# Optimization experiments

Hardware: AMD Instinct MI355X
Metric: run time of the kernel (lower is better)

Reference implementation:

```python
import jax, jax.numpy as jnp
import numpy as np

EPS = 1e-9

def _cheb_attention_conv(X_real, X_imag, lap_real, lap_imag,
                         Wa_real, Wa_imag, ba_real, ba_imag,
                         modrelu_b, W_real, W_imag):
    B, N, C = X_real.shape
    # --- attention scores: CVLinear over cat([x_i, x_j]) == (X@W1)_i + (X@W2)_j + b ---
    W1r, W2r = Wa_real[:C, 0], Wa_real[C:, 0]  # [C]
    W1i, W2i = Wa_imag[:C, 0], Wa_imag[C:, 0]
    # complex matvec: (Xr + iXi)(Wr + iWi)
    si_r = X_real @ W1r - X_imag @ W1i          # [B,N] contribution of x_i
    si_i = X_real @ W1i + X_imag @ W1r
    sj_r = X_real @ W2r - X_imag @ W2i          # [B,N] contribution of x_j
    sj_i = X_real @ W2i + X_imag @ W2r
    sc_r = si_r[:, :, None] + sj_r[:, None, :] + ba_real[0]   # [B,N,N]
    sc_i = si_i[:, :, None] + sj_i[:, None, :] + ba_imag[0]
    # --- learnable modReLU: relu(|z| + b) * z/|z| ---
    mag = jnp.sqrt(sc_r * sc_r + sc_i * sc_i)
    scale = jax.nn.relu(mag + modrelu_b[0]) / (mag + EPS)
    sc_r = sc_r * scale
    sc_i = sc_i * scale
    # --- split complex softmax over last dim ---
    a_r = jax.nn.softmax(sc_r, axis=-1)
    a_i = jax.nn.softmax(sc_i, axis=-1)
    # --- reweight Laplacian polynomials (complex mult, broadcast over k) ---
    L_r = lap_real * a_r[:, None] - lap_imag * a_i[:, None]   # [B,K+1,N,N]
    L_i = lap_real * a_i[:, None] + lap_imag * a_r[:, None]
    # --- sum_k (L_k X) W_k, complex ---
    LX_r = jnp.einsum('bkij,bjc->bkic', L_r, X_real) - jnp.einsum('bkij,bjc->bkic', L_i, X_imag)
    LX_i = jnp.einsum('bkij,bjc->bkic', L_r, X_imag) + jnp.einsum('bkij,bjc->bkic', L_i, X_real)
    out_r = jnp.einsum('bkic,kco->bio', LX_r, W_real) - jnp.einsum('bkic,kco->bio', LX_i, W_imag)
    out_i = jnp.einsum('bkic,kco->bio', LX_r, W_imag) + jnp.einsum('bkic,kco->bio', LX_i, W_real)
    return out_r, out_i


def setup_inputs() -> dict:
    key = jax.random.key(0)
    ks = jax.random.split(key, 8)
    B, N, C, CO, K1 = 48, 512, 64, 64, 5
    # weights normalized to unit complex magnitude like the torch init
    wr = jax.random.uniform(ks[4], (K1, C, CO), minval=-1.0, maxval=1.0) / np.sqrt(CO)
    wi = jax.random.uniform(ks[5], (K1, C, CO), minval=-1.0, maxval=1.0) / np.sqrt(CO)
    m = jnp.sqrt(wr * wr + wi * wi)
    return {
        'X_real': jax.random.normal(ks[0], (B, N, C), jnp.float32),
        'X_imag': jax.random.normal(ks[1], (B, N, C), jnp.float32),
        'lap_real': jax.random.normal(ks[2], (B, K1, N, N), jnp.float32) * 0.1,
        'lap_imag': jax.random.normal(ks[3], (B, K1, N, N), jnp.float32) * 0.1,
        'Wa_real': jax.random.normal(ks[6], (2 * C, 1), jnp.float32) * 0.1,
        'Wa_imag': jax.random.normal(ks[7], (2 * C, 1), jnp.float32) * 0.1,
        'ba_real': jnp.zeros((1,), jnp.float32),
        'ba_imag': jnp.zeros((1,), jnp.float32),
        'modrelu_b': jnp.zeros((1,), jnp.float32),
        'W_real': (wr / m).astype(jnp.float32),
        'W_imag': (wi / m).astype(jnp.float32),
    }


def reference(X_real, X_imag, lap_real, lap_imag, Wa_real, Wa_imag,
              ba_real, ba_imag, modrelu_b, W_real, W_imag):
    out_r, out_i = _cheb_attention_conv(X_real, X_imag, lap_real, lap_imag,
                                        Wa_real, Wa_imag, ba_real, ba_imag,
                                        modrelu_b, W_real, W_imag)
    return out_r, out_i
```

## Files before the change

### kernel.cpp

```cpp
#include <hip/hip_runtime.h>

#define EPSF 1e-9f

typedef __attribute__((ext_vector_type(8))) short short8;
typedef __attribute__((ext_vector_type(4))) float f32x4;
typedef __attribute__((ext_vector_type(4))) unsigned int u32x4;
typedef __attribute__((ext_vector_type(2))) unsigned int u32x2;

__device__ __forceinline__ unsigned pkbf(float lo, float hi) {
  unsigned r;
  asm("v_cvt_pk_bf16_f32 %0, %1, %2" : "=v"(r) : "v"(lo), "v"(hi));
  return r;
}
__device__ __forceinline__ short8 mk8(unsigned a, unsigned b, unsigned c, unsigned d) {
  u32x4 u = {a, b, c, d};
  return __builtin_bit_cast(short8, u);
}

__global__ __launch_bounds__(256) void k_s(
    const float* __restrict__ Xr, const float* __restrict__ Xi,
    const float* __restrict__ War, const float* __restrict__ Wai,
    float4* __restrict__ s4, float2* __restrict__ sj2)
{
  int t = threadIdx.x;
  int nf = blockIdx.x * 32 + (t >> 3);
  int c0 = (t & 7) * 8;
  const f32x4* xr = (const f32x4*)(Xr + (size_t)nf * 64 + c0);
  const f32x4* xi = (const f32x4*)(Xi + (size_t)nf * 64 + c0);
  const f32x4* w1r = (const f32x4*)(War + c0);
  const f32x4* w2r = (const f32x4*)(War + 64 + c0);
  const f32x4* w1i = (const f32x4*)(Wai + c0);
  const f32x4* w2i = (const f32x4*)(Wai + 64 + c0);
  float sir = 0.f, sii = 0.f, sjr = 0.f, sji = 0.f;
#pragma unroll
  for (int h = 0; h < 2; ++h) {
    f32x4 a = xr[h], bb = xi[h];
    f32x4 u1r = w1r[h], u1i = w1i[h], u2r = w2r[h], u2i = w2i[h];
#pragma unroll
    for (int e = 0; e < 4; ++e) {
      sir += a[e] * u1r[e] - bb[e] * u1i[e];
      sii += a[e] * u1i[e] + bb[e] * u1r[e];
      sjr += a[e] * u2r[e] - bb[e] * u2i[e];
      sji += a[e] * u2i[e] + bb[e] * u2r[e];
    }
  }
#pragma unroll
  for (int off = 1; off < 8; off <<= 1) {
    sir += __shfl_xor(sir, off);
    sii += __shfl_xor(sii, off);
    sjr += __shfl_xor(sjr, off);
    sji += __shfl_xor(sji, off);
  }
  if ((t & 7) == 0) {
    s4[nf] = make_float4(sir, sii, sjr, sji);
    sj2[nf] = make_float2(sjr, sji);
  }
}

__global__ __launch_bounds__(256) void k_stats(
    const float4* __restrict__ s4, const float2* __restrict__ sj2,
    const float* __restrict__ bar, const float* __restrict__ bai,
    const float* __restrict__ modbp, float4* __restrict__ stats)
{
  __shared__ float2 sh[512];
  int t = threadIdx.x;
  int b = blockIdx.x >> 4;
  int i0 = (blockIdx.x & 15) * 32;
  sh[t] = sj2[(size_t)b * 512 + t];
  sh[t + 256] = sj2[(size_t)b * 512 + t + 256];
  __syncthreads();
  float ba_r = bar[0], ba_i = bai[0], modb = modbp[0];
  int i = i0 + (t >> 3), jl = t & 7;
  float4 sv = s4[(size_t)b * 512 + i];
  float sirb = sv.x + ba_r, siib = sv.y + ba_i;
  float mr = -1e30f, mi = -1e30f;
  for (int jj = 0; jj < 64; ++jj) {
    float2 sj = sh[jl * 64 + jj];
    float scr = sirb + sj.x, sci = siib + sj.y;
    float mag = sqrtf(scr * scr + sci * sci);
    float sc = fmaxf(mag + modb, 0.f) * __builtin_amdgcn_rcpf(mag + EPSF);
    mr = fmaxf(mr, scr * sc);
    mi = fmaxf(mi, sci * sc);
  }
#pragma unroll
  for (int off = 1; off < 8; off <<= 1) {
    mr = fmaxf(mr, __shfl_xor(mr, off));
    mi = fmaxf(mi, __shfl_xor(mi, off));
  }
  float er = 0.f, ei = 0.f;
  for (int jj = 0; jj < 64; ++jj) {
    float2 sj = sh[jl * 64 + jj];
    float scr = sirb + sj.x, sci = siib + sj.y;
    float mag = sqrtf(scr * scr + sci * sci);
    float sc = fmaxf(mag + modb, 0.f) * __builtin_amdgcn_rcpf(mag + EPSF);
    er += __expf(scr * sc - mr);
    ei += __expf(sci * sc - mi);
  }
#pragma unroll
  for (int off = 1; off < 8; off <<= 1) {
    er += __shfl_xor(er, off);
    ei += __shfl_xor(ei, off);
  }
  if (jl == 0)
    stats[(size_t)b * 512 + i] = make_float4(mr, 1.f / er, mi, 1.f / ei);
}

__global__ __launch_bounds__(256) void k_y(
    const float* __restrict__ Xr, const float* __restrict__ Xi,
    const float* __restrict__ Wr, const float* __restrict__ Wi,
    u32x4* __restrict__ yfrag)
{
  __shared__ __align__(16) short WtR[64 * 72];
  __shared__ __align__(16) short WtI[64 * 72];
  __shared__ __align__(16) short Yt[4][2][64 * 24];
  int bk = blockIdx.x;
  int b = bk / 5, k = bk % 5;
  int t = threadIdx.x;
  {
    int o = t & 63, cbase = (t >> 6) * 16;
    const float* wr = Wr + (size_t)k * 4096;
    const float* wi = Wi + (size_t)k * 4096;
#pragma unroll
    for (int cc = 0; cc < 16; cc += 2) {
      int c = cbase + cc;
      *(unsigned*)&WtR[o * 72 + c] = pkbf(wr[c * 64 + o], wr[(c + 1) * 64 + o]);
      *(unsigned*)&WtI[o * 72 + c] = pkbf(wi[c * 64 + o], wi[(c + 1) * 64 + o]);
    }
  }
  __syncthreads();
  int w = t >> 6, l = t & 63;
  int lane15 = l & 15, quad = l >> 4;
  short* ytR = &Yt[w][0][0];
  short* ytI = &Yt[w][1][0];
  for (int qq = 0; qq < 8; ++qq) {
    int q = w * 8 + qq;
    int j = q * 16 + lane15;
    const f32x4* pxr = (const f32x4*)(Xr + ((size_t)b * 512 + j) * 64 + quad * 8);
    const f32x4* pxi = (const f32x4*)(Xi + ((size_t)b * 512 + j) * 64 + quad * 8);
    f32x4 xr0 = pxr[0], xr1 = pxr[1], xr8 = pxr[8], xr9 = pxr[9];
    f32x4 xi0 = pxi[0], xi1 = pxi[1], xi8 = pxi[8], xi9 = pxi[9];
    short8 axr[2], axi[2];
    axr[0] = mk8(pkbf(xr0[0], xr0[1]), pkbf(xr0[2], xr0[3]), pkbf(xr1[0], xr1[1]), pkbf(xr1[2], xr1[3]));
    axr[1] = mk8(pkbf(xr8[0], xr8[1]), pkbf(xr8[2], xr8[3]), pkbf(xr9[0], xr9[1]), pkbf(xr9[2], xr9[3]));
    axi[0] = mk8(pkbf(xi0[0], xi0[1]), pkbf(xi0[2], xi0[3]), pkbf(xi1[0], xi1[1]), pkbf(xi1[2], xi1[3]));
    axi[1] = mk8(pkbf(xi8[0], xi8[1]), pkbf(xi8[2], xi8[3]), pkbf(xi9[0], xi9[1]), pkbf(xi9[2], xi9[3]));
    f32x4 aR1[4], aR2[4], aI[4];
#pragma unroll
    for (int os = 0; os < 4; ++os) {
      aR1[os] = f32x4{0.f, 0.f, 0.f, 0.f};
      aR2[os] = f32x4{0.f, 0.f, 0.f, 0.f};
      aI[os] = f32x4{0.f, 0.f, 0.f, 0.f};
    }
#pragma unroll
    for (int kc = 0; kc < 2; ++kc) {
#pragma unroll
      for (int os = 0; os < 4; ++os) {
        int widx = (os * 16 + lane15) * 72 + kc * 32 + quad * 8;
        short8 wrF = *(const short8*)&WtR[widx];
        short8 wiF = *(const short8*)&WtI[widx];
        aR1[os] = __builtin_amdgcn_mfma_f32_16x16x32_bf16(axr[kc], wrF, aR1[os], 0, 0, 0);
        aR2[os] = __builtin_amdgcn_mfma_f32_16x16x32_bf16(axi[kc], wiF, aR2[os], 0, 0, 0);
        aI[os]  = __builtin_amdgcn_mfma_f32_16x16x32_bf16(axr[kc], wiF, aI[os], 0, 0, 0);
        aI[os]  = __builtin_amdgcn_mfma_f32_16x16x32_bf16(axi[kc], wrF, aI[os], 0, 0, 0);
      }
    }
#pragma unroll
    for (int os = 0; os < 4; ++os) {
      f32x4 R = aR1[os] - aR2[os];
      f32x4 I = aI[os];
      int ya = (os * 16 + lane15) * 24 + quad * 4;
      *(u32x2*)&ytR[ya] = u32x2{pkbf(R[0], R[1]), pkbf(R[2], R[3])};
      *(u32x2*)&ytI[ya] = u32x2{pkbf(I[0], I[1]), pkbf(I[2], I[3])};
    }
#pragma unroll
    for (int part = 0; part < 2; ++part) {
      const short* yt = part ? ytI : ytR;
#pragma unroll
      for (int h = 0; h < 2; ++h) {
        short8 unit = *(const short8*)&yt[l * 24 + h * 8];
        size_t line = (((size_t)(b * 5 + k) * 2 + part) * 16 + (q >> 1)) * 4 + (l >> 4);
        size_t idx = line * 64 + ((q & 1) * 2 + h) * 16 + (l & 15);
        yfrag[idx] = __builtin_bit_cast(u32x4, unit);
      }
    }
  }
}

__global__ __launch_bounds__(256) __attribute__((amdgpu_waves_per_eu(2, 2)))
void k_main(
    const float* __restrict__ lapr, const float* __restrict__ lapi,
    const float4* __restrict__ s4, const float4* __restrict__ stats,
    const float2* __restrict__ sj2, const u32x4* __restrict__ yfrag,
    const float* __restrict__ bar, const float* __restrict__ bai,
    const float* __restrict__ modbp,
    float* __restrict__ out_r, float* __restrict__ out_i)
{
  __shared__ __align__(16) f32x4 red[2][64][8];

  const int g = blockIdx.x;
  const int b = (g & 7) + ((g >> 8) << 3);
  const int it = (g >> 3) & 31;
  const int t = threadIdx.x;
  const int w = t >> 6;
  const int l = t & 63;
  const int lane15 = l & 15, quad = l >> 4;
  const int gi = it * 16 + lane15;

  float ba_r = bar[0], ba_i = bai[0], modb = modbp[0];
  float4 sv = s4[(size_t)b * 512 + gi];
  float4 st = stats[(size_t)b * 512 + gi];
  float sirb = sv.x + ba_r, siib = sv.y + ba_i;
  float maxr = st.x, rsr = st.y, maxi = st.z, rsi = st.w;

  f32x4 accR[4], accI[4];
#pragma unroll
  for (int os = 0; os < 4; ++os) {
    accR[os] = f32x4{0.f, 0.f, 0.f, 0.f};
    accI[os] = f32x4{0.f, 0.f, 0.f, 0.f};
  }

  const size_t NN = (size_t)512 * 512;
  const float* lapr_b = lapr + ((size_t)b * 5 * 512 + gi) * 512;
  const float* lapi_b = lapi + ((size_t)b * 5 * 512 + gi) * 512;
  const u32x4* yb = yfrag + (size_t)b * 5 * 8192 + l;

  for (int jsw = 0; jsw < 4; ++jsw) {
    const int js = w * 4 + jsw;
    const int jq = js * 32 + quad * 8;

    const f32x4* sjp = (const f32x4*)(sj2 + (size_t)b * 512 + jq);
    f32x4 sjv0 = sjp[0], sjv1 = sjp[1], sjv2 = sjp[2], sjv3 = sjp[3];

    f32x4 LR[5][2], LI[5][2];
#pragma unroll
    for (int k = 0; k < 5; ++k) {
      const f32x4* pr = (const f32x4*)(lapr_b + (size_t)k * NN + jq);
      const f32x4* pi_ = (const f32x4*)(lapi_b + (size_t)k * NN + jq);
      LR[k][0] = __builtin_nontemporal_load(pr);
      LR[k][1] = __builtin_nontemporal_load(pr + 1);
      LI[k][0] = __builtin_nontemporal_load(pi_);
      LI[k][1] = __builtin_nontemporal_load(pi_ + 1);
    }
    __builtin_amdgcn_sched_barrier(0);

    float sjr[8] = {sjv0[0], sjv0[2], sjv1[0], sjv1[2], sjv2[0], sjv2[2], sjv3[0], sjv3[2]};
    float sjimag[8] = {sjv0[1], sjv0[3], sjv1[1], sjv1[3], sjv2[1], sjv2[3], sjv3[1], sjv3[3]};
    float ar[8], ai[8];
#pragma unroll
    for (int e = 0; e < 8; ++e) {
      float scr = sirb + sjr[e];
      float sci = siib + sjimag[e];
      float mag = __builtin_amdgcn_sqrtf(fmaf(scr, scr, sci * sci));
      float sc = fmaxf(mag + modb, 0.f) * __builtin_amdgcn_rcpf(mag + EPSF);
      ar[e] = __expf(fmaf(scr, sc, -maxr)) * rsr;
      ai[e] = __expf(fmaf(sci, sc, -maxi)) * rsi;
    }

#pragma unroll
    for (int k = 0; k < 5; ++k) {
      float lrv[8], liv[8];
#pragma unroll
      for (int e = 0; e < 4; ++e) {
        lrv[e]     = LR[k][0][e] * ar[e]     - LI[k][0][e] * ai[e];
        liv[e]     = LR[k][0][e] * ai[e]     + LI[k][0][e] * ar[e];
        lrv[4 + e] = LR[k][1][e] * ar[4 + e] - LI[k][1][e] * ai[4 + e];
        liv[4 + e] = LR[k][1][e] * ai[4 + e] + LI[k][1][e] * ar[4 + e];
      }
      unsigned p0 = pkbf(lrv[0], lrv[1]), p1 = pkbf(lrv[2], lrv[3]);
      unsigned p2 = pkbf(lrv[4], lrv[5]), p3 = pkbf(lrv[6], lrv[7]);
      unsigned q0 = pkbf(liv[0], liv[1]), q1 = pkbf(liv[2], liv[3]);
      unsigned q2 = pkbf(liv[4], liv[5]), q3 = pkbf(liv[6], liv[7]);
      short8 Ar = mk8(p0, p1, p2, p3);
      short8 Ai = mk8(q0, q1, q2, q3);
      short8 An = mk8(q0 ^ 0x80008000u, q1 ^ 0x80008000u,
                      q2 ^ 0x80008000u, q3 ^ 0x80008000u);

      const u32x4* yk = yb + (size_t)k * 8192 + (size_t)(js * 4) * 64;
#pragma unroll
      for (int os = 0; os < 4; ++os) {
        short8 br8 = __builtin_bit_cast(short8, yk[os * 64]);
        short8 bi8 = __builtin_bit_cast(short8, yk[4096 + os * 64]);
        accR[os] = __builtin_amdgcn_mfma_f32_16x16x32_bf16(Ar, br8, accR[os], 0, 0, 0);
        accR[os] = __builtin_amdgcn_mfma_f32_16x16x32_bf16(An, bi8, accR[os], 0, 0, 0);
        accI[os] = __builtin_amdgcn_mfma_f32_16x16x32_bf16(Ar, bi8, accI[os], 0, 0, 0);
        accI[os] = __builtin_amdgcn_mfma_f32_16x16x32_bf16(Ai, br8, accI[os], 0, 0, 0);
      }
    }
  }

  if (w >= 2) {
#pragma unroll
    for (int os = 0; os < 4; ++os) {
      red[w - 2][l][os] = accR[os];
      red[w - 2][l][4 + os] = accI[os];
    }
  }
  __syncthreads();
  if (w < 2) {
#pragma unroll
    for (int os = 0; os < 4; ++os) {
      accR[os] += red[w][l][os];
      accI[os] += red[w][l][4 + os];
    }
  }
  __syncthreads();
  if (w == 1) {
#pragma unroll
    for (int os = 0; os < 4; ++os) {
      red[0][l][os] = accR[os];
      red[0][l][4 + os] = accI[os];
    }
  }
  __syncthreads();
  if (w == 0) {
#pragma unroll
    for (int os = 0; os < 4; ++os) {
      accR[os] += red[0][l][os];
      accI[os] += red[0][l][4 + os];
      int oc = os * 16 + lane15;
#pragma unroll
      for (int r = 0; r < 4; ++r) {
        size_t oidx = ((size_t)b * 512 + it * 16 + quad * 4 + r) * 64 + oc;
        out_r[oidx] = accR[os][r];
        out_i[oidx] = accI[os][r];
      }
    }
  }
}

extern "C" void kernel_launch(void* const* d_in, const int* in_sizes, int n_in,
                              void* d_out, int out_size, void* d_ws, size_t ws_size,
                              hipStream_t stream) {
  const float* Xr = (const float*)d_in[0];
  const float* Xi = (const float*)d_in[1];
  const float* lapr = (const float*)d_in[2];
  const float* lapi = (const float*)d_in[3];
  const float* War = (const float*)d_in[4];
  const float* Wai = (const float*)d_in[5];
  const float* bar = (const float*)d_in[6];
  const float* bai = (const float*)d_in[7];
  const float* modb = (const float*)d_in[8];
  const float* Wr = (const float*)d_in[9];
  const float* Wi = (const float*)d_in[10];

  char* wsb = (char*)d_ws;
  float4* s4 = (float4*)wsb;
  float4* stats = (float4*)(wsb + 393216);
  float2* sj2 = (float2*)(wsb + 786432);
  u32x4* yfrag = (u32x4*)(wsb + 983040);

  float* out_r = (float*)d_out;
  float* out_i = out_r + (size_t)48 * 512 * 64;

  k_s<<<768, 256, 0, stream>>>(Xr, Xi, War, Wai, s4, sj2);
  k_stats<<<768, 256, 0, stream>>>(s4, sj2, bar, bai, modb, stats);
  k_y<<<240, 256, 0, stream>>>(Xr, Xi, Wr, Wi, yfrag);
  k_main<<<1536, 256, 0, stream>>>(lapr, lapi, s4, stats, sj2, yfrag,
                                   bar, bai, modb, out_r, out_i);
}
```

Before: 190.8 us.

## Relax waves-per-eu, use plain Laplacian loads, and make reduction buffer scalar-strided

Three unrelated tweaks to the main kernel. The waves_per_eu attribute goes from (2,2) to (2,8), so the compiler may use fewer registers and allow more resident waves. The Laplacian loads switch from nontemporal to ordinary cached loads. The shared-memory reduction buffer becomes a scalar-per-lane layout, trading wide 16-byte LDS accesses for conflict-free 4-byte ones. Higher occupancy could add register pressure or spills, and cached loads may pollute the cache for streamed data.

```diff
diff --git a/kernel.cpp b/kernel.cpp
--- a/kernel.cpp
+++ b/kernel.cpp
@@ -186,7 +186,7 @@
   }
 }
 
-__global__ __launch_bounds__(256) __attribute__((amdgpu_waves_per_eu(2, 2)))
+__global__ __launch_bounds__(256) __attribute__((amdgpu_waves_per_eu(2, 8)))
 void k_main(
     const float* __restrict__ lapr, const float* __restrict__ lapi,
     const float4* __restrict__ s4, const float4* __restrict__ stats,
@@ -195,7 +195,7 @@
     const float* __restrict__ modbp,
     float* __restrict__ out_r, float* __restrict__ out_i)
 {
-  __shared__ __align__(16) f32x4 red[2][64][8];
+  __shared__ float red[2][2][4][4][64];
 
   const int g = blockIdx.x;
   const int b = (g & 7) + ((g >> 8) << 3);
@@ -236,10 +236,10 @@
     for (int k = 0; k < 5; ++k) {
       const f32x4* pr = (const f32x4*)(lapr_b + (size_t)k * NN + jq);
       const f32x4* pi_ = (const f32x4*)(lapi_b + (size_t)k * NN + jq);
-      LR[k][0] = __builtin_nontemporal_load(pr);
-      LR[k][1] = __builtin_nontemporal_load(pr + 1);
-      LI[k][0] = __builtin_nontemporal_load(pi_);
-      LI[k][1] = __builtin_nontemporal_load(pi_ + 1);
+      LR[k][0] = pr[0];
+      LR[k][1] = pr[1];
+      LI[k][0] = pi_[0];
+      LI[k][1] = pi_[1];
     }
     __builtin_amdgcn_sched_barrier(0);
 
@@ -290,33 +290,42 @@
 
   if (w >= 2) {
 #pragma unroll
+    for (int os = 0; os < 4; ++os)
+#pragma unroll
+      for (int c = 0; c < 4; ++c) {
+        red[w - 2][0][os][c][l] = accR[os][c];
+        red[w - 2][1][os][c][l] = accI[os][c];
+      }
+  }
+  __syncthreads();
+  if (w < 2) {
+#pragma unroll
+    for (int os = 0; os < 4; ++os)
+#pragma unroll
+      for (int c = 0; c < 4; ++c) {
+        accR[os][c] += red[w][0][os][c][l];
+        accI[os][c] += red[w][1][os][c][l];
+      }
+  }
+  __syncthreads();
+  if (w == 1) {
+#pragma unroll
+    for (int os = 0; os < 4; ++os)
+#pragma unroll
+      for (int c = 0; c < 4; ++c) {
+        red[0][0][os][c][l] = accR[os][c];
+        red[0][1][os][c][l] = accI[os][c];
+      }
+  }
+  __syncthreads();
+  if (w == 0) {
+#pragma unroll
     for (int os = 0; os < 4; ++os) {
-      red[w - 2][l][os] = accR[os];
-      red[w - 2][l][4 + os] = accI[os];
-    }
-  }
-  __syncthreads();
-  if (w < 2) {
-#pragma unroll
-    for (int os = 0; os < 4; ++os) {
-      accR[os] += red[w][l][os];
-      accI[os] += red[w][l][4 + os];
-    }
-  }
-  __syncthreads();
-  if (w == 1) {
-#pragma unroll
-    for (int os = 0; os < 4; ++os) {
-      red[0][l][os] = accR[os];
-      red[0][l][4 + os] = accI[os];
-    }
-  }
-  __syncthreads();
-  if (w == 0) {
-#pragma unroll
-    for (int os = 0; os < 4; ++os) {
-      accR[os] += red[0][l][os];
-      accI[os] += red[0][l][4 + os];
+#pragma unroll
+      for (int c = 0; c < 4; ++c) {
+        accR[os][c] += red[0][0][os][c][l];
+        accI[os][c] += red[0][1][os][c][l];
+      }
       int oc = os * 16 + lane15;
 #pragma unroll
       for (int r = 0; r < 4; ++r) {
```

Result: slower. 222.6 us (+16.7%).
